# Performance work log

Measured on AMD Instinct MI355X. Metric: run time of the kernel, lower is better.

Reference implementation:

```python
import jax, jax.numpy as jnp
import numpy as np

B, D_IN, D_HID, D_OUT = 16384, 512, 512, 512
E, K = 8, 2
VQ_COEFF, LB_COEFF = 0.05, 0.01
LOG100 = float(np.log(100.0))
LOG2 = float(np.log(2.0))


def _normalize(v):
    # torch F.normalize(dim=1): x / max(||x||, 1e-12)
    n = jnp.linalg.norm(v, axis=-1, keepdims=True)
    return v / jnp.maximum(n, 1e-12)


def _cv_squared(v):
    # torch .var() is unbiased (ddof=1)
    return jnp.var(v, ddof=1) / (jnp.mean(v) ** 2 + 1e-10)


def _rbm_layer(x, rm, W, b, ca, temp):
    # x: [B, d_in], rm: [E, d_in], W: [E, d_out, d_in], b: [E, d_out]
    rm_n = jax.lax.stop_gradient(_normalize(rm))          # .detach() in source
    nx = _normalize(x)
    dists = nx @ rm_n.T                                    # [B, E]
    top_v, top_i = jax.lax.top_k(dists, K)                 # [B, K]
    tv = jax.nn.softmax(top_v, axis=-1)                    # softmax over top-k
    bsz = dists.shape[0]
    attn = jnp.zeros_like(dists).at[jnp.arange(bsz)[:, None], top_i].set(tv)
    # const_attention is frozen (requires_grad=False)
    inp_att = jnp.exp(jnp.minimum(jax.lax.stop_gradient(ca), LOG100))  # [E]
    # dense gather-compute-scatter: expert e output for every token, masked by attn
    eo = jnp.einsum('bi,eoi->beo', x, W) * inp_att[None, :, None] + b[None, :, :]
    out = jnp.einsum('be,beo->bo', jax.lax.stop_gradient(attn), eo)    # att.detach()
    out = out * jnp.exp(jnp.minimum(temp, LOG100))
    # aux losses (eval mode: no EMA memory update)
    vq = -(nx[:, None, :] * rm_n[top_i]).sum(-1)           # [B, K]
    vq_loss = (tv * vq).sum(-1).mean()
    lb = _cv_squared(attn.sum(0))
    aux = VQ_COEFF * vq_loss + LB_COEFF * lb               # sim_coeff = 0
    return out, aux


def setup_inputs() -> dict:
    key = jax.random.key(0)
    ks = jax.random.split(key, 8)
    x = jax.random.normal(ks[0], (B, D_IN), dtype=jnp.float32)
    rm0 = _normalize(jax.random.normal(ks[1], (E, D_IN), dtype=jnp.float32))
    W0 = jax.random.normal(ks[2], (E, D_HID, D_IN), dtype=jnp.float32) / np.sqrt(D_IN)
    b0 = jnp.zeros((E, D_HID), dtype=jnp.float32)
    rm1 = _normalize(jax.random.normal(ks[3], (E, D_HID), dtype=jnp.float32))
    W1 = jax.random.normal(ks[4], (E, D_OUT, D_HID), dtype=jnp.float32) / np.sqrt(D_HID)
    b1 = jnp.zeros((E, D_OUT), dtype=jnp.float32)
    temp0 = jnp.full((1,), LOG2, dtype=jnp.float32)
    temp1 = jnp.full((1,), LOG2, dtype=jnp.float32)
    ca0 = jnp.zeros((E,), dtype=jnp.float32)
    ca1 = jnp.zeros((E,), dtype=jnp.float32)
    return {"x": x, "rm0": rm0, "W0": W0, "b0": b0, "temp0": temp0, "ca0": ca0,
            "rm1": rm1, "W1": W1, "b1": b1, "temp1": temp1, "ca1": ca1}


def reference(x, rm0, W0, b0, temp0, ca0, rm1, W1, b1, temp1, ca1):
    h0, a0 = _rbm_layer(x, rm0, W0, b0, ca0, temp0)
    h_emb = h0                      # embedding tapped after layer 0 (pre-activation)
    h = jax.nn.relu(h0)             # norm_type=None -> no norm
    h1, a1 = _rbm_layer(h, rm1, W1, b1, ca1, temp1)
    return (h_emb, h1, a0 + a1)
```

## Files before the change

kernel.cpp:

```cpp
#include <hip/hip_runtime.h>
#include <cmath>
#include <cstdint>

#define NTOK   16384
#define DM     512
#define NEXP   8
#define LOG100 4.605170185988092f

typedef _Float16 half8  __attribute__((ext_vector_type(8)));
typedef _Float16 half4  __attribute__((ext_vector_type(4)));
typedef float    floatx4 __attribute__((ext_vector_type(4)));

#define MFMA_F16(a, b, c) __builtin_amdgcn_mfma_f32_16x16x32_f16((a), (b), (c), 0, 0, 0)

__device__ __forceinline__ void gl_lds16(const void* g, void* l) {
    __builtin_amdgcn_global_load_lds(
        (const __attribute__((address_space(1))) void*)g,
        (__attribute__((address_space(3))) void*)l, 16, 0, 0);
}


__global__ __launch_bounds__(256) void prep_kernel(
    const float* __restrict__ rm0, const float* __restrict__ rm1,
    const float* __restrict__ ca0, const float* __restrict__ ca1,
    const float* __restrict__ temp0, const float* __restrict__ temp1,
    float* __restrict__ ctrl, float* __restrict__ rmn)
{
    int tid = threadIdx.x, lane = tid & 63, w = tid >> 6;
    if (tid < 32) ((int*)ctrl)[tid] = 0;
    if (tid >= 32 && tid < 48) ctrl[tid] = 0.f;
    if (tid == 48 || tid == 49) ctrl[tid] = 0.f;
    if (tid == 50) ctrl[50] = expf(fminf(temp0[0], LOG100));
    if (tid == 51) ctrl[51] = expf(fminf(temp1[0], LOG100));
    if (tid >= 52 && tid < 68) {
        int i = tid - 52;
        ctrl[tid] = expf(fminf(i < 8 ? ca0[i] : ca1[i - 8], LOG100));
    }
    for (int r = w; r < 16; r += 4) {
        const float* src = (r < 8) ? (rm0 + r * DM) : (rm1 + (r - 8) * DM);
        float v[8]; float ss = 0.f;
        #pragma unroll
        for (int j = 0; j < 8; ++j) { v[j] = src[lane + 64 * j]; ss += v[j] * v[j]; }
        #pragma unroll
        for (int off = 32; off > 0; off >>= 1) ss += __shfl_xor(ss, off);
        float inv = 1.f / fmaxf(sqrtf(ss), 1e-12f);
        float* dst = rmn + r * DM;
        #pragma unroll
        for (int j = 0; j < 8; ++j) dst[lane + 64 * j] = v[j] * inv;
    }
}

__global__ __launch_bounds__(256) void conv_w_kernel(
    const float4* __restrict__ W0, const float4* __restrict__ W1,
    half4* __restrict__ w0hi, half4* __restrict__ w0lo, half4* __restrict__ w1h)
{
    int i = blockIdx.x * 256 + threadIdx.x;
    float4 a = W0[i], b = W1[i];
    const float* ap = (const float*)&a;
    const float* bp = (const float*)&b;
    half4 hi, lo, h1;
    #pragma unroll
    for (int j = 0; j < 4; ++j) {
        _Float16 h = (_Float16)ap[j];
        hi[j] = h;
        lo[j] = (_Float16)(ap[j] - (float)h);
        h1[j] = (_Float16)bp[j];
    }
    w0hi[i] = hi; w0lo[i] = lo; w1h[i] = h1;
}

__global__ __launch_bounds__(256) void route_kernel(
    const float* __restrict__ src,
    const float* __restrict__ rmn,
    int relu_in,
    _Float16* __restrict__ dst_hi,
    _Float16* __restrict__ dst_lo,
    unsigned char* __restrict__ key,
    float2* __restrict__ wts,
    float2* __restrict__ bs)
{
    __shared__ float rmLds[NEXP * DM];
    int tid = threadIdx.x;
    for (int i = tid; i < NEXP * DM; i += 256) rmLds[i] = rmn[i];
    __syncthreads();
    int lane = tid & 63, w = tid >> 6;
    int token = blockIdx.x * 4 + w;

    const float* row = src + (size_t)token * DM;
    float x[8]; float ss = 0.f;
    #pragma unroll
    for (int j = 0; j < 8; ++j) {
        float v = row[lane + 64 * j];
        if (relu_in) v = fmaxf(v, 0.f);
        x[j] = v; ss += v * v;
    }
    #pragma unroll
    for (int j = 0; j < 8; ++j) {
        _Float16 h = (_Float16)x[j];
        dst_hi[(size_t)token * DM + lane + 64 * j] = h;
        if (dst_lo) dst_lo[(size_t)token * DM + lane + 64 * j] = (_Float16)(x[j] - (float)h);
    }
    float d[8];
    #pragma unroll
    for (int e = 0; e < 8; ++e) {
        float a = 0.f;
        #pragma unroll
        for (int j = 0; j < 8; ++j) a += x[j] * rmLds[e * DM + lane + 64 * j];
        d[e] = a;
    }
    #pragma unroll
    for (int off = 32; off > 0; off >>= 1) {
        ss += __shfl_xor(ss, off);
        #pragma unroll
        for (int e = 0; e < 8; ++e) d[e] += __shfl_xor(d[e], off);
    }
    float inv = 1.f / fmaxf(sqrtf(ss), 1e-12f);
    float best = -1e30f, second = -1e30f; int be = 0, se = 0;
    #pragma unroll
    for (int e = 0; e < 8; ++e) {
        float de = d[e] * inv;
        if (de > best)        { second = best; se = be; best = de; be = e; }
        else if (de > second) { second = de; se = e; }
    }
    float z = expf(second - best);
    float w0 = 1.f / (1.f + z), w1 = z / (1.f + z);
    if (lane == 0) {
        key[token] = (unsigned char)be;
        key[NTOK + token] = (unsigned char)se;
        wts[token] = make_float2(w0, w1);
        bs[token] = make_float2(best, second);
    }
}

__global__ __launch_bounds__(256) void compact_kernel(
    const unsigned char* __restrict__ key,
    const float2* __restrict__ wts,
    const float2* __restrict__ bs,
    int* __restrict__ cnt,
    unsigned short* __restrict__ bkt,
    float* __restrict__ imp,
    float* __restrict__ vq_acc)
{
    int slot = blockIdx.x >> 3, e = blockIdx.x & 7;
    const unsigned char* k = key + slot * NTOK;
    unsigned short* ob = bkt + (size_t)(slot * 8 + e) * NTOK;
    __shared__ int wc[2][4];
    int tid = threadIdx.x, lane = tid & 63, w = tid >> 6;
    int base = 0;
    float wsum = 0.f, vqs = 0.f;
    for (int c = 0; c < 64; ++c) {
        int tok = c * 256 + tid;
        bool m = (k[tok] == (unsigned char)e);
        unsigned long long mask = __ballot(m);
        int p = c & 1;
        if (lane == 0) wc[p][w] = __popcll(mask);
        __syncthreads();
        int off = base;
        for (int i = 0; i < w; ++i) off += wc[p][i];
        if (m) {
            int pre = __popcll(mask & ((1ull << lane) - 1ull));
            ob[off + pre] = (unsigned short)tok;
            float2 wp = wts[tok]; float2 b2 = bs[tok];
            float wv = slot ? wp.y : wp.x;
            wsum += wv;
            vqs  += wv * (slot ? b2.y : b2.x);
        }
        base += wc[p][0] + wc[p][1] + wc[p][2] + wc[p][3];
    }
    #pragma unroll
    for (int off = 32; off > 0; off >>= 1) {
        wsum += __shfl_xor(wsum, off);
        vqs  += __shfl_xor(vqs, off);
    }
    __shared__ float rw[4], rv[4];
    if (lane == 0) { rw[w] = wsum; rv[w] = vqs; }
    __syncthreads();
    if (tid == 0) {
        cnt[slot * 8 + e] = base;
        float W = rw[0] + rw[1] + rw[2] + rw[3];
        float V = rv[0] + rv[1] + rv[2] + rv[3];
        atomicAdd(&imp[e], W);
        atomicAdd(vq_acc, -V);
    }
}

template <bool SPLIT>
__global__ __launch_bounds__(256) void gemm_kernel(
    const _Float16* __restrict__ Ahi, const _Float16* __restrict__ Alo,
    const _Float16* __restrict__ Whi, const _Float16* __restrict__ Wlo,
    const float* __restrict__ bias,
    const float* __restrict__ iav,
    const float* __restrict__ tscp,
    const int* __restrict__ cnt,
    const unsigned short* __restrict__ bkt,
    const float2* __restrict__ wts,
    int slot, int accum,
    float* __restrict__ outp)
{
    __shared__ __align__(16) _Float16 lds[2 * 128 * 64];
    __shared__ int tokLds[128];
    _Float16* tA = lds;
    _Float16* tB = lds + 128 * 64;

    int e = blockIdx.x >> 7, mt = blockIdx.x & 127;
    int M = cnt[e];
    int m0 = mt << 7;
    if (m0 >= M) return;
    int n0 = blockIdx.y << 7;
    int valid = min(128, M - m0);
    int tid = threadIdx.x, lane = tid & 63, w = tid >> 6;
    if (tid < 128) tokLds[tid] = bkt[e * NTOK + m0 + min(tid, valid - 1)];
    __syncthreads();

    floatx4 acc[4][4];
    #pragma unroll
    for (int mi = 0; mi < 4; ++mi)
        #pragma unroll
        for (int ni = 0; ni < 4; ++ni) acc[mi][ni] = (floatx4){0.f, 0.f, 0.f, 0.f};

    const _Float16* WbH = Whi + ((size_t)e * DM + n0) * DM;
    const _Float16* WbL = SPLIT ? (Wlo + ((size_t)e * DM + n0) * DM) : nullptr;

    int subRow = lane >> 3, p = lane & 7;
    int cSt = p ^ (subRow & 7);
    int wm = w >> 1, wn = w & 1;
    int r0 = wm * 64, c0 = wn * 64;
    int q = lane >> 4, l15 = lane & 15;

    constexpr int KIT = SPLIT ? 16 : 8;
    constexpr int KSTEP = SPLIT ? 32 : 64;

    for (int kb = 0; kb < KIT; ++kb) {
        int k0 = kb * KSTEP;
        #pragma unroll
        for (int j = w; j < 16; j += 4) {
            int row = j * 8 + subRow;
            int tok = tokLds[row];
            const _Float16* g;
            if constexpr (SPLIT)
                g = (cSt < 4) ? (Ahi + (size_t)tok * DM + k0 + cSt * 8)
                              : (Alo + (size_t)tok * DM + k0 + (cSt - 4) * 8);
            else
                g = Ahi + (size_t)tok * DM + k0 + cSt * 8;
            gl_lds16(g, (void*)(tA + j * 512));
        }
        #pragma unroll
        for (int j = w; j < 16; j += 4) {
            int row = j * 8 + subRow;
            const _Float16* g;
            if constexpr (SPLIT)
                g = (cSt < 4) ? (WbH + (size_t)row * DM + k0 + cSt * 8)
                              : (WbL + (size_t)row * DM + k0 + (cSt - 4) * 8);
            else
                g = WbH + (size_t)row * DM + k0 + cSt * 8;
            gl_lds16(g, (void*)(tB + j * 512));
        }
        __syncthreads();

        if constexpr (SPLIT) {
            half8 ah[4], al[4];
            #pragma unroll
            for (int mi = 0; mi < 4; ++mi) {
                int r = r0 + mi * 16 + l15;
                int ph = q ^ (r & 7), pl = (q + 4) ^ (r & 7);
                ah[mi] = *(const half8*)(tA + r * 64 + ph * 8);
                al[mi] = *(const half8*)(tA + r * 64 + pl * 8);
            }
            #pragma unroll
            for (int ni = 0; ni < 4; ++ni) {
                int r = c0 + ni * 16 + l15;
                int ph = q ^ (r & 7), pl = (q + 4) ^ (r & 7);
                half8 bh = *(const half8*)(tB + r * 64 + ph * 8);
                half8 bl = *(const half8*)(tB + r * 64 + pl * 8);
                #pragma unroll
                for (int mi = 0; mi < 4; ++mi) acc[mi][ni] = MFMA_F16(ah[mi], bh, acc[mi][ni]);
                #pragma unroll
                for (int mi = 0; mi < 4; ++mi) acc[mi][ni] = MFMA_F16(ah[mi], bl, acc[mi][ni]);
                #pragma unroll
                for (int mi = 0; mi < 4; ++mi) acc[mi][ni] = MFMA_F16(al[mi], bh, acc[mi][ni]);
            }
        } else {
            #pragma unroll
            for (int ks = 0; ks < 2; ++ks) {
                half8 a[4];
                #pragma unroll
                for (int mi = 0; mi < 4; ++mi) {
                    int r = r0 + mi * 16 + l15;
                    int pc = (ks * 4 + q) ^ (r & 7);
                    a[mi] = *(const half8*)(tA + r * 64 + pc * 8);
                }
                #pragma unroll
                for (int ni = 0; ni < 4; ++ni) {
                    int r = c0 + ni * 16 + l15;
                    int pc = (ks * 4 + q) ^ (r & 7);
                    half8 b = *(const half8*)(tB + r * 64 + pc * 8);
                    #pragma unroll
                    for (int mi = 0; mi < 4; ++mi) acc[mi][ni] = MFMA_F16(a[mi], b, acc[mi][ni]);
                }
            }
        }
        __syncthreads();
    }

    float t = *tscp, iae = iav[e];
    float bv[4];
    #pragma unroll
    for (int ni = 0; ni < 4; ++ni) bv[ni] = bias[e * DM + n0 + c0 + ni * 16 + l15];
    #pragma unroll
    for (int mi = 0; mi < 4; ++mi) {
        int liBase = r0 + mi * 16 + q * 4;
        #pragma unroll
        for (int reg = 0; reg < 4; ++reg) {
            int li = liBase + reg;
            if (li < valid) {
                int tok = tokLds[li];
                float2 wp = wts[tok];
                float wgt = slot ? wp.y : wp.x;
                float sg = t * wgt * iae, sb = t * wgt;
                float* orow = outp + (size_t)tok * DM + n0;
                #pragma unroll
                for (int ni = 0; ni < 4; ++ni) {
                    float v = acc[mi][ni][reg] * sg + bv[ni] * sb;
                    int c = c0 + ni * 16 + l15;
                    if (accum) orow[c] += v; else orow[c] = v;
                }
            }
        }
    }
}

__global__ void finalize_kernel(const float* __restrict__ ctrl, float* __restrict__ outp)
{
    if (threadIdx.x == 0) {
        float aux = 0.f;
        for (int l = 0; l < 2; ++l) {
            float vq = ctrl[48 + l] / (float)NTOK;
            float mean = 0.f;
            for (int e = 0; e < 8; ++e) mean += ctrl[32 + l * 8 + e];
            mean *= 0.125f;
            float s = 0.f;
            for (int e = 0; e < 8; ++e) {
                float d = ctrl[32 + l * 8 + e] - mean;
                s += d * d;
            }
            float var = s / 7.f;
            float lb = var / (mean * mean + 1e-10f);
            aux += 0.05f * vq + 0.01f * lb;
        }
        *outp = aux;
    }
}

extern "C" void kernel_launch(void* const* d_in, const int* in_sizes, int n_in,
                              void* d_out, int out_size, void* d_ws, size_t ws_size,
                              hipStream_t stream) {
    const float* x     = (const float*)d_in[0];
    const float* rm0   = (const float*)d_in[1];
    const float* W0    = (const float*)d_in[2];
    const float* b0    = (const float*)d_in[3];
    const float* temp0 = (const float*)d_in[4];
    const float* ca0   = (const float*)d_in[5];
    const float* rm1   = (const float*)d_in[6];
    const float* W1    = (const float*)d_in[7];
    const float* b1    = (const float*)d_in[8];
    const float* temp1 = (const float*)d_in[9];
    const float* ca1   = (const float*)d_in[10];
    float* out = (float*)d_out;

    char* ws = (char*)d_ws;
    float* ctrl = (float*)ws;
    int*   cnt  = (int*)ctrl;
    float* imp  = ctrl + 32;
    float* vq   = ctrl + 48;
    float* tsc  = ctrl + 50;
    float* ia   = ctrl + 52;
    float* rmn  = ctrl + 128;
    float2*        wts = (float2*)(ws + (size_t)64  * 1024);
    float2*        bs  = (float2*)(ws + (size_t)384 * 1024);
    unsigned char* key = (unsigned char*)(ws + (size_t)704 * 1024);

    char* big = ws + (1 << 20);
    half4*          w0hi4 = (half4*)(big);
    half4*          w0lo4 = (half4*)(big + (size_t)4  * 1024 * 1024);
    half4*          w1h4  = (half4*)(big + (size_t)8  * 1024 * 1024);
    _Float16*       w0hi  = (_Float16*)w0hi4;
    _Float16*       w0lo  = (_Float16*)w0lo4;
    _Float16*       w1h   = (_Float16*)w1h4;
    _Float16*       h16   = (_Float16*)(big + (size_t)12 * 1024 * 1024);
    unsigned short* bkt   = (unsigned short*)(big + (size_t)28 * 1024 * 1024);

    _Float16* xhi = (_Float16*)(out + (size_t)NTOK * DM);
    _Float16* xlo = xhi + (size_t)NTOK * DM;

    prep_kernel<<<1, 256, 0, stream>>>(rm0, rm1, ca0, ca1, temp0, temp1, ctrl, rmn);
    conv_w_kernel<<<2048, 256, 0, stream>>>((const float4*)W0, (const float4*)W1,
                                            w0hi4, w0lo4, w1h4);

    route_kernel<<<4096, 256, 0, stream>>>(x, rmn, 0, xhi, xlo,
        key, wts, bs);
    compact_kernel<<<16, 256, 0, stream>>>(key, wts, bs, cnt, bkt, imp, vq);
    gemm_kernel<true><<<dim3(1024, 4), 256, 0, stream>>>(xhi, xlo, w0hi, w0lo, b0, ia, tsc,
        cnt, bkt, wts, 0, 0, out);
    gemm_kernel<true><<<dim3(1024, 4), 256, 0, stream>>>(xhi, xlo, w0hi, w0lo, b0, ia, tsc,
        cnt + 8, bkt + 8 * NTOK, wts, 1, 1, out);

    route_kernel<<<4096, 256, 0, stream>>>(out, rmn + 4096, 1, h16, (_Float16*)nullptr,
        key + 2 * NTOK, wts + NTOK, bs + NTOK);
    compact_kernel<<<16, 256, 0, stream>>>(key + 2 * NTOK, wts + NTOK, bs + NTOK,
        cnt + 16, bkt + 16 * NTOK, imp + 8, vq + 1);
    gemm_kernel<false><<<dim3(1024, 4), 256, 0, stream>>>(h16, (const _Float16*)nullptr, w1h,
        (const _Float16*)nullptr, b1, ia + 8, tsc + 1,
        cnt + 16, bkt + 16 * NTOK, wts + NTOK, 0, 0, out + (size_t)NTOK * DM);
    gemm_kernel<false><<<dim3(1024, 4), 256, 0, stream>>>(h16, (const _Float16*)nullptr, w1h,
        (const _Float16*)nullptr, b1, ia + 8, tsc + 1,
        cnt + 24, bkt + 24 * NTOK, wts + NTOK, 1, 1, out + (size_t)NTOK * DM);

    finalize_kernel<<<1, 64, 0, stream>>>(ctrl, out + (size_t)2 * NTOK * DM);
}
```

Baseline: 488.4 us.

## Double-buffer grouped GEMM and prepack weights/activations into tile-contiguous swizzled layout

Weights are prepacked into a per-tile layout that already carries the XOR swizzle, and the hi/lo fp16 halves are interleaved. Layer-0 activations are written with hi and lo interleaved per 32-column chunk, so every global-to-LDS load is a contiguous 16-byte fetch. The GEMM now double-buffers LDS so the next K-block loads while the current one computes, and it remaps block indices so the expert dimension is interleaved across the grid. This targets load latency and scattered address math, at the cost of twice the LDS per block, which may lower occupancy.

New measurement: 530.7 us. 8.6% more time.

```diff
diff --git a/kernel.cpp b/kernel.cpp
--- a/kernel.cpp
+++ b/kernel.cpp
@@ -8,7 +8,6 @@
 #define LOG100 4.605170185988092f
 
 typedef _Float16 half8  __attribute__((ext_vector_type(8)));
-typedef _Float16 half4  __attribute__((ext_vector_type(4)));
 typedef float    floatx4 __attribute__((ext_vector_type(4)));
 
 #define MFMA_F16(a, b, c) __builtin_amdgcn_mfma_f32_16x16x32_f16((a), (b), (c), 0, 0, 0)
@@ -50,31 +49,44 @@
     }
 }
 
-__global__ __launch_bounds__(256) void conv_w_kernel(
-    const float4* __restrict__ W0, const float4* __restrict__ W1,
-    half4* __restrict__ w0hi, half4* __restrict__ w0lo, half4* __restrict__ w1h)
+__global__ __launch_bounds__(256) void pack_w_kernel(
+    const float* __restrict__ W0, const float* __restrict__ W1,
+    half8* __restrict__ w0pk, half8* __restrict__ w1pk)
 {
     int i = blockIdx.x * 256 + threadIdx.x;
-    float4 a = W0[i], b = W1[i];
-    const float* ap = (const float*)&a;
-    const float* bp = (const float*)&b;
-    half4 hi, lo, h1;
-    #pragma unroll
-    for (int j = 0; j < 4; ++j) {
-        _Float16 h = (_Float16)ap[j];
-        hi[j] = h;
-        lo[j] = (_Float16)(ap[j] - (float)h);
-        h1[j] = (_Float16)bp[j];
-    }
-    w0hi[i] = hi; w0lo[i] = lo; w1h[i] = h1;
+    if (i < 512 * 1024) {
+        int l = i & 63, j = (i >> 6) & 15, kb = (i >> 10) & 15, nt = (i >> 14) & 3, e = i >> 16;
+        int s = l >> 3, p = l & 7, c = p ^ s;
+        int n = nt * 128 + j * 8 + s;
+        int k = kb * 32 + (c & 3) * 8;
+        const float* src = W0 + ((size_t)e * DM + n) * DM + k;
+        half8 v;
+        #pragma unroll
+        for (int t = 0; t < 8; ++t) {
+            float f = src[t];
+            _Float16 h = (_Float16)f;
+            v[t] = (c < 4) ? h : (_Float16)(f - (float)h);
+        }
+        w0pk[i] = v;
+    } else {
+        int m = i - 512 * 1024;
+        int l = m & 63, j = (m >> 6) & 15, kb = (m >> 10) & 7, nt = (m >> 13) & 3, e = m >> 15;
+        int s = l >> 3, p = l & 7, c = p ^ s;
+        int n = nt * 128 + j * 8 + s;
+        int k = kb * 64 + c * 8;
+        const float* src = W1 + ((size_t)e * DM + n) * DM + k;
+        half8 v;
+        #pragma unroll
+        for (int t = 0; t < 8; ++t) v[t] = (_Float16)src[t];
+        w1pk[m] = v;
+    }
 }
 
 __global__ __launch_bounds__(256) void route_kernel(
     const float* __restrict__ src,
     const float* __restrict__ rmn,
-    int relu_in,
-    _Float16* __restrict__ dst_hi,
-    _Float16* __restrict__ dst_lo,
+    int relu_in, int split,
+    _Float16* __restrict__ dst,
     unsigned char* __restrict__ key,
     float2* __restrict__ wts,
     float2* __restrict__ bs)
@@ -94,11 +106,19 @@
         if (relu_in) v = fmaxf(v, 0.f);
         x[j] = v; ss += v * v;
     }
-    #pragma unroll
-    for (int j = 0; j < 8; ++j) {
-        _Float16 h = (_Float16)x[j];
-        dst_hi[(size_t)token * DM + lane + 64 * j] = h;
-        if (dst_lo) dst_lo[(size_t)token * DM + lane + 64 * j] = (_Float16)(x[j] - (float)h);
+    if (split) {
+        #pragma unroll
+        for (int j = 0; j < 8; ++j) {
+            int k = lane + 64 * j;
+            size_t base = (size_t)token * 1024 + (size_t)((k >> 5) << 6) + (k & 31);
+            _Float16 h = (_Float16)x[j];
+            dst[base] = h;
+            dst[base + 32] = (_Float16)(x[j] - (float)h);
+        }
+    } else {
+        #pragma unroll
+        for (int j = 0; j < 8; ++j)
+            dst[(size_t)token * DM + lane + 64 * j] = (_Float16)x[j];
     }
     float d[8];
     #pragma unroll
@@ -186,8 +206,8 @@
 
 template <bool SPLIT>
 __global__ __launch_bounds__(256) void gemm_kernel(
-    const _Float16* __restrict__ Ahi, const _Float16* __restrict__ Alo,
-    const _Float16* __restrict__ Whi, const _Float16* __restrict__ Wlo,
+    const _Float16* __restrict__ A,
+    const _Float16* __restrict__ Wpk,
     const float* __restrict__ bias,
     const float* __restrict__ iav,
     const float* __restrict__ tscp,
@@ -197,81 +217,75 @@
     int slot, int accum,
     float* __restrict__ outp)
 {
-    __shared__ __align__(16) _Float16 lds[2 * 128 * 64];
+    __shared__ __align__(16) _Float16 lds[2 * 16384];
     __shared__ int tokLds[128];
-    _Float16* tA = lds;
-    _Float16* tB = lds + 128 * 64;
-
-    int e = blockIdx.x >> 7, mt = blockIdx.x & 127;
+
+    int bx = ((blockIdx.x & 7) << 7) | (blockIdx.x >> 3);
+    int e = bx >> 7, mt = bx & 127;
     int M = cnt[e];
     int m0 = mt << 7;
     if (m0 >= M) return;
-    int n0 = blockIdx.y << 7;
+    int nt = blockIdx.y, n0 = nt << 7;
     int valid = min(128, M - m0);
     int tid = threadIdx.x, lane = tid & 63, w = tid >> 6;
     if (tid < 128) tokLds[tid] = bkt[e * NTOK + m0 + min(tid, valid - 1)];
     __syncthreads();
 
-    floatx4 acc[4][4];
-    #pragma unroll
-    for (int mi = 0; mi < 4; ++mi)
-        #pragma unroll
-        for (int ni = 0; ni < 4; ++ni) acc[mi][ni] = (floatx4){0.f, 0.f, 0.f, 0.f};
-
-    const _Float16* WbH = Whi + ((size_t)e * DM + n0) * DM;
-    const _Float16* WbL = SPLIT ? (Wlo + ((size_t)e * DM + n0) * DM) : nullptr;
-
     int subRow = lane >> 3, p = lane & 7;
-    int cSt = p ^ (subRow & 7);
+    int cSt = p ^ subRow;
     int wm = w >> 1, wn = w & 1;
     int r0 = wm * 64, c0 = wn * 64;
     int q = lane >> 4, l15 = lane & 15;
 
     constexpr int KIT = SPLIT ? 16 : 8;
-    constexpr int KSTEP = SPLIT ? 32 : 64;
-
-    for (int kb = 0; kb < KIT; ++kb) {
-        int k0 = kb * KSTEP;
-        #pragma unroll
-        for (int j = w; j < 16; j += 4) {
-            int row = j * 8 + subRow;
-            int tok = tokLds[row];
-            const _Float16* g;
-            if constexpr (SPLIT)
-                g = (cSt < 4) ? (Ahi + (size_t)tok * DM + k0 + cSt * 8)
-                              : (Alo + (size_t)tok * DM + k0 + (cSt - 4) * 8);
-            else
-                g = Ahi + (size_t)tok * DM + k0 + cSt * 8;
-            gl_lds16(g, (void*)(tA + j * 512));
-        }
-        #pragma unroll
-        for (int j = w; j < 16; j += 4) {
-            int row = j * 8 + subRow;
-            const _Float16* g;
-            if constexpr (SPLIT)
-                g = (cSt < 4) ? (WbH + (size_t)row * DM + k0 + cSt * 8)
-                              : (WbL + (size_t)row * DM + k0 + (cSt - 4) * 8);
-            else
-                g = WbH + (size_t)row * DM + k0 + cSt * 8;
-            gl_lds16(g, (void*)(tB + j * 512));
-        }
-        __syncthreads();
-
+    constexpr int AS  = SPLIT ? 1024 : 512;
+
+    int tokR[4];
+    #pragma unroll
+    for (int jj = 0; jj < 4; ++jj) tokR[jj] = tokLds[(w + jj * 4) * 8 + subRow];
+
+    const _Float16* wtile = Wpk + (size_t)(e * 4 + nt) * KIT * 8192;
+
+    floatx4 acc[4][4];
+    #pragma unroll
+    for (int mi = 0; mi < 4; ++mi)
+        #pragma unroll
+        for (int ni = 0; ni < 4; ++ni) acc[mi][ni] = (floatx4){0.f, 0.f, 0.f, 0.f};
+
+    auto stage = [&](int kb, int buf) {
+        _Float16* dA = lds + buf * 16384;
+        _Float16* dB = dA + 8192;
+        #pragma unroll
+        for (int jj = 0; jj < 4; ++jj) {
+            int j = w + jj * 4;
+            gl_lds16(A + (size_t)tokR[jj] * AS + kb * 64 + cSt * 8, (void*)(dA + j * 512));
+        }
+        const _Float16* wb = wtile + (size_t)kb * 8192;
+        #pragma unroll
+        for (int jj = 0; jj < 4; ++jj) {
+            int j = w + jj * 4;
+            gl_lds16(wb + j * 512 + lane * 8, (void*)(dB + j * 512));
+        }
+    };
+
+    auto compute = [&](int buf) {
+        const _Float16* bA = lds + buf * 16384;
+        const _Float16* bB = bA + 8192;
         if constexpr (SPLIT) {
             half8 ah[4], al[4];
             #pragma unroll
             for (int mi = 0; mi < 4; ++mi) {
                 int r = r0 + mi * 16 + l15;
                 int ph = q ^ (r & 7), pl = (q + 4) ^ (r & 7);
-                ah[mi] = *(const half8*)(tA + r * 64 + ph * 8);
-                al[mi] = *(const half8*)(tA + r * 64 + pl * 8);
+                ah[mi] = *(const half8*)(bA + r * 64 + ph * 8);
+                al[mi] = *(const half8*)(bA + r * 64 + pl * 8);
             }
             #pragma unroll
             for (int ni = 0; ni < 4; ++ni) {
                 int r = c0 + ni * 16 + l15;
                 int ph = q ^ (r & 7), pl = (q + 4) ^ (r & 7);
-                half8 bh = *(const half8*)(tB + r * 64 + ph * 8);
-                half8 bl = *(const half8*)(tB + r * 64 + pl * 8);
+                half8 bh = *(const half8*)(bB + r * 64 + ph * 8);
+                half8 bl = *(const half8*)(bB + r * 64 + pl * 8);
                 #pragma unroll
                 for (int mi = 0; mi < 4; ++mi) acc[mi][ni] = MFMA_F16(ah[mi], bh, acc[mi][ni]);
                 #pragma unroll
@@ -287,20 +301,30 @@
                 for (int mi = 0; mi < 4; ++mi) {
                     int r = r0 + mi * 16 + l15;
                     int pc = (ks * 4 + q) ^ (r & 7);
-                    a[mi] = *(const half8*)(tA + r * 64 + pc * 8);
+                    a[mi] = *(const half8*)(bA + r * 64 + pc * 8);
                 }
                 #pragma unroll
                 for (int ni = 0; ni < 4; ++ni) {
                     int r = c0 + ni * 16 + l15;
                     int pc = (ks * 4 + q) ^ (r & 7);
-                    half8 b = *(const half8*)(tB + r * 64 + pc * 8);
+                    half8 b = *(const half8*)(bB + r * 64 + pc * 8);
                     #pragma unroll
                     for (int mi = 0; mi < 4; ++mi) acc[mi][ni] = MFMA_F16(a[mi], b, acc[mi][ni]);
                 }
             }
         }
+    };
+
+    stage(0, 0);
+    __syncthreads();
+    int cur = 0;
+    for (int kb = 0; kb < KIT - 1; ++kb) {
+        stage(kb + 1, cur ^ 1);
+        compute(cur);
         __syncthreads();
-    }
+        cur ^= 1;
+    }
+    compute(cur);
 
     float t = *tscp, iae = iav[e];
     float bv[4];
@@ -380,39 +404,32 @@
     unsigned char* key = (unsigned char*)(ws + (size_t)704 * 1024);
 
     char* big = ws + (1 << 20);
-    half4*          w0hi4 = (half4*)(big);
-    half4*          w0lo4 = (half4*)(big + (size_t)4  * 1024 * 1024);
-    half4*          w1h4  = (half4*)(big + (size_t)8  * 1024 * 1024);
-    _Float16*       w0hi  = (_Float16*)w0hi4;
-    _Float16*       w0lo  = (_Float16*)w0lo4;
-    _Float16*       w1h   = (_Float16*)w1h4;
+    half8*          w0pk8 = (half8*)(big);
+    half8*          w1pk8 = (half8*)(big + (size_t)8  * 1024 * 1024);
+    const _Float16* w0pk  = (const _Float16*)w0pk8;
+    const _Float16* w1pk  = (const _Float16*)w1pk8;
     _Float16*       h16   = (_Float16*)(big + (size_t)12 * 1024 * 1024);
     unsigned short* bkt   = (unsigned short*)(big + (size_t)28 * 1024 * 1024);
 
-    _Float16* xhi = (_Float16*)(out + (size_t)NTOK * DM);
-    _Float16* xlo = xhi + (size_t)NTOK * DM;
+    _Float16* xpk = (_Float16*)(out + (size_t)NTOK * DM);
 
     prep_kernel<<<1, 256, 0, stream>>>(rm0, rm1, ca0, ca1, temp0, temp1, ctrl, rmn);
-    conv_w_kernel<<<2048, 256, 0, stream>>>((const float4*)W0, (const float4*)W1,
-                                            w0hi4, w0lo4, w1h4);
-
-    route_kernel<<<4096, 256, 0, stream>>>(x, rmn, 0, xhi, xlo,
-        key, wts, bs);
+    pack_w_kernel<<<3072, 256, 0, stream>>>(W0, W1, w0pk8, w1pk8);
+
+    route_kernel<<<4096, 256, 0, stream>>>(x, rmn, 0, 1, xpk, key, wts, bs);
     compact_kernel<<<16, 256, 0, stream>>>(key, wts, bs, cnt, bkt, imp, vq);
-    gemm_kernel<true><<<dim3(1024, 4), 256, 0, stream>>>(xhi, xlo, w0hi, w0lo, b0, ia, tsc,
+    gemm_kernel<true><<<dim3(1024, 4), 256, 0, stream>>>(xpk, w0pk, b0, ia, tsc,
         cnt, bkt, wts, 0, 0, out);
-    gemm_kernel<true><<<dim3(1024, 4), 256, 0, stream>>>(xhi, xlo, w0hi, w0lo, b0, ia, tsc,
+    gemm_kernel<true><<<dim3(1024, 4), 256, 0, stream>>>(xpk, w0pk, b0, ia, tsc,
         cnt + 8, bkt + 8 * NTOK, wts, 1, 1, out);
 
-    route_kernel<<<4096, 256, 0, stream>>>(out, rmn + 4096, 1, h16, (_Float16*)nullptr,
+    route_kernel<<<4096, 256, 0, stream>>>(out, rmn + 4096, 1, 0, h16,
         key + 2 * NTOK, wts + NTOK, bs + NTOK);
     compact_kernel<<<16, 256, 0, stream>>>(key + 2 * NTOK, wts + NTOK, bs + NTOK,
         cnt + 16, bkt + 16 * NTOK, imp + 8, vq + 1);
-    gemm_kernel<false><<<dim3(1024, 4), 256, 0, stream>>>(h16, (const _Float16*)nullptr, w1h,
-        (const _Float16*)nullptr, b1, ia + 8, tsc + 1,
+    gemm_kernel<false><<<dim3(1024, 4), 256, 0, stream>>>(h16, w1pk, b1, ia + 8, tsc + 1,
         cnt + 16, bkt + 16 * NTOK, wts + NTOK, 0, 0, out + (size_t)NTOK * DM);
-    gemm_kernel<false><<<dim3(1024, 4), 256, 0, stream>>>(h16, (const _Float16*)nullptr, w1h,
-        (const _Float16*)nullptr, b1, ia + 8, tsc + 1,
+    gemm_kernel<false><<<dim3(1024, 4), 256, 0, stream>>>(h16, w1pk, b1, ia + 8, tsc + 1,
         cnt + 24, bkt + 24 * NTOK, wts + NTOK, 1, 1, out + (size_t)NTOK * DM);
 
     finalize_kernel<<<1, 64, 0, stream>>>(ctrl, out + (size_t)2 * NTOK * DM);
```
